# Kernel tuning notes

Hardware: AMD Instinct MI355X
Metric: run time of the kernel (lower is better)

Reference implementation:

```python
import jax, jax.numpy as jnp
import numpy as np

N = 200_000   # nodes per component
E = 400_000   # directed edges per component
F_IN = 32     # raw node features
H = 96        # hidden_dim / GatedGraphConv out_channels
L = 6         # num_layers inside GatedGraphConv
B = 4096      # number of molecules (graphs) in batch
FC = 4 * H    # 384


def _gru_cell(m, h, w_ih, w_hh, b_ih, b_hh):
    # torch.nn.GRUCell math; w_* are [3H, H], b_* are [3H]
    gi = m @ w_ih.T + b_ih
    gh = h @ w_hh.T + b_hh
    i_r, i_z, i_n = jnp.split(gi, 3, axis=1)
    h_r, h_z, h_n = jnp.split(gh, 3, axis=1)
    r = jax.nn.sigmoid(i_r + h_r)
    z = jax.nn.sigmoid(i_z + h_z)
    n = jnp.tanh(i_n + r * h_n)
    return (1.0 - z) * n + z * h


def _gated_graph_conv(x, edge_index, W, w_ih, w_hh, b_ih, b_hh):
    n_nodes = x.shape[0]
    h = jnp.pad(x, ((0, 0), (0, H - x.shape[1])))  # pad features to H
    src, dst = edge_index[0], edge_index[1]        # message flows src -> dst
    for i in range(L):
        m = h @ W[i]                                # [N, H]
        agg = jax.ops.segment_sum(m[src], dst, num_segments=n_nodes)
        h = _gru_cell(agg, h, w_ih, w_hh, b_ih, b_hh)
    return h


def _pool_component(x, edge_index, batch, W, w_ih, w_hh, b_ih, b_hh):
    h = jax.nn.relu(_gated_graph_conv(x, edge_index, W, w_ih, w_hh, b_ih, b_hh))
    sums = jax.ops.segment_sum(h, batch, num_segments=B)
    cnt = jax.ops.segment_sum(jnp.ones((h.shape[0], 1), h.dtype), batch, num_segments=B)
    return sums / jnp.maximum(cnt, 1.0)            # global_mean_pool -> [B, H]


def setup_inputs() -> dict:
    key = jax.random.key(0)
    ks = jax.random.split(key, 16)
    d = {}
    for i in range(3):
        c = str(i + 1)
        kx, ke, kb = jax.random.split(ks[i], 3)
        d['x' + c] = jax.random.normal(kx, (N, F_IN), jnp.float32)
        d['edge_index' + c] = jax.random.randint(ke, (2, E), 0, N)
        d['batch' + c] = jnp.sort(jax.random.randint(kb, (N,), 0, B))
        kw = jax.random.split(ks[3 + i], 5)
        d['W' + c] = jax.random.normal(kw[0], (L, H, H), jnp.float32) * 0.05
        d['wih' + c] = jax.random.normal(kw[1], (3 * H, H), jnp.float32) * 0.05
        d['whh' + c] = jax.random.normal(kw[2], (3 * H, H), jnp.float32) * 0.05
        d['bih' + c] = jax.random.normal(kw[3], (3 * H,), jnp.float32) * 0.05
        d['bhh' + c] = jax.random.normal(kw[4], (3 * H,), jnp.float32) * 0.05
    kf = jax.random.split(ks[7], 6)
    d['fc1_w'] = jax.random.normal(kf[0], (FC, FC * 4), jnp.float32) * 0.05
    d['fc1_b'] = jnp.zeros((FC * 4,), jnp.float32)
    d['fc2_w'] = jax.random.normal(kf[1], (FC * 4, FC), jnp.float32) * 0.05
    d['fc2_b'] = jnp.zeros((FC,), jnp.float32)
    d['fc3_w'] = jax.random.normal(kf[2], (FC, 3), jnp.float32) * 0.05
    d['fc3_b'] = jnp.zeros((3,), jnp.float32)
    return d


def reference(x1, edge_index1, batch1, x2, edge_index2, batch2, x3, edge_index3, batch3,
              W1, wih1, whh1, bih1, bhh1,
              W2, wih2, whh2, bih2, bhh2,
              W3, wih3, whh3, bih3, bhh3,
              fc1_w, fc1_b, fc2_w, fc2_b, fc3_w, fc3_b):
    g1 = _pool_component(x1, edge_index1, batch1, W1, wih1, whh1, bih1, bhh1)
    g2 = _pool_component(x2, edge_index2, batch2, W2, wih2, whh2, bih2, bhh2)
    g3 = _pool_component(x3, edge_index3, batch3, W3, wih3, whh3, bih3, bhh3)
    xx = g1 * g2 * g3
    x = jnp.concatenate((g1, g2, g3, xx), axis=1)   # [B, 4H]
    x = jax.nn.relu(x @ fc1_w + fc1_b)              # dropout is identity (eval)
    x = jax.nn.relu(x @ fc2_w + fc2_b)
    return x @ fc3_w + fc3_b                        # [B, 3]
```

## Files before the change

kernel.cpp:

```cpp
#include <hip/hip_runtime.h>
#include <math.h>

#define NN_ 200000
#define EE_ 400000
#define HH  96
#define LL  6
#define BB  4096
#define NT_ 12500
#define SCAN_B 1024
#define NB_SCAN 196

typedef short s8v __attribute__((ext_vector_type(8)));
typedef float f4v __attribute__((ext_vector_type(4)));
typedef float f2v __attribute__((ext_vector_type(2)));

static inline int cdiv(int a, int b) { return (a + b - 1) / b; }

__device__ __forceinline__ float sigmoidf_(float x) { return 1.0f / (1.0f + __expf(-x)); }
__device__ __forceinline__ float tanhf_(float x) { return 1.0f - 2.0f / (__expf(2.0f * x) + 1.0f); }
__device__ __forceinline__ unsigned short f2bf(float x) {
    unsigned u = __float_as_uint(x);
    unsigned r = u + 0x7FFF + ((u >> 16) & 1);
    return (unsigned short)(r >> 16);
}
__device__ __forceinline__ float bf2f(unsigned short u) {
    return __uint_as_float(((unsigned)u) << 16);
}
__device__ __forceinline__ s8v load_bf8(const float* __restrict__ p) {
    float4 v0 = *(const float4*)p;
    float4 v1 = *(const float4*)(p + 4);
    s8v r;
    r[0] = (short)f2bf(v0.x); r[1] = (short)f2bf(v0.y);
    r[2] = (short)f2bf(v0.z); r[3] = (short)f2bf(v0.w);
    r[4] = (short)f2bf(v1.x); r[5] = (short)f2bf(v1.y);
    r[6] = (short)f2bf(v1.z); r[7] = (short)f2bf(v1.w);
    return r;
}

__device__ __forceinline__ void accu_(f2v& a, unsigned u) {
    a[0] += __uint_as_float(u << 16);
    a[1] += __uint_as_float(u & 0xFFFF0000u);
}
__device__ __forceinline__ void acc_row_(f2v* ag2, const uint4& u, int ks) {
    accu_(ag2[ks * 4 + 0], u.x); accu_(ag2[ks * 4 + 1], u.y);
    accu_(ag2[ks * 4 + 2], u.z); accu_(ag2[ks * 4 + 3], u.w);
}

__global__ void packB_k(const float* __restrict__ B, unsigned short* __restrict__ Bp,
                        int K, int N)
{
    int idx = blockIdx.x * 256 + threadIdx.x;
    if (idx >= K * N) return;
    int k = idx / N, n = idx % N;
    Bp[(((size_t)(k >> 5) * N + n) * 4 + ((k >> 3) & 3)) * 8 + (k & 7)] = f2bf(B[idx]);
}

__global__ void packWp_k(const float* __restrict__ W, unsigned short* __restrict__ Wp)
{
    int idx = blockIdx.x * 256 + threadIdx.x;
    if (idx >= LL * 6 * 3 * 64 * 8) return;
    int j    = idx & 7;
    int lane = (idx >> 3) & 63;
    int rest = idx >> 9;
    int ks = rest % 3;
    int jb = (rest / 3) % 6;
    int l  = rest / 18;
    int quad = lane >> 4, lc = lane & 15;
    int k = ks * 32 + quad * 8 + j;
    int n = jb * 16 + lc;
    Wp[idx] = f2bf(W[(size_t)l * 9216 + (size_t)k * 96 + n]);
}

__global__ void packWgc_k(const float* __restrict__ wih, const float* __restrict__ whh,
                          unsigned short* __restrict__ Wgc)
{
    int idx = blockIdx.x * 256 + threadIdx.x;
    if (idx >= 6 * 18 * 64 * 8) return;
    int j    = idx & 7;
    int lane = (idx >> 3) & 63;
    int rest = idx >> 9;
    int ksb = rest % 18;
    int jb  = rest / 18;
    int quad = lane >> 4, lc = lane & 15;
    int g, ks;
    if (ksb < 6)       { g = 0; ks = ksb; }
    else if (ksb < 12) { g = 1; ks = ksb - 6; }
    else if (ksb < 15) { g = 2; ks = ksb - 12; }
    else               { g = 3; ks = ksb - 12; }
    int k = ks * 32 + quad * 8 + j;
    int n = g * 96 + jb * 16 + lc;
    float v;
    if (n < 192) {
        v = (k < 96) ? wih[(size_t)n * 96 + k] : whh[(size_t)n * 96 + (k - 96)];
    } else if (n < 288) {
        int jj = n - 192;
        v = wih[(size_t)(192 + jj) * 96 + k];
    } else {
        int jj = n - 288;
        v = whh[(size_t)(192 + jj) * 96 + (k - 96)];
    }
    Wgc[idx] = f2bf(v);
}

__global__ void bpack_k(const float* __restrict__ bih, const float* __restrict__ bhh,
                        float* __restrict__ bs)
{
    int j = threadIdx.x;
    if (j >= 96) return;
    bs[j]        = bih[j] + bhh[j];
    bs[96 + j]   = bih[96 + j] + bhh[96 + j];
    bs[192 + j]  = bih[192 + j];
    bs[288 + j]  = bhh[192 + j];
}

__global__ void pad_k(const float* __restrict__ x, unsigned short* __restrict__ hbf)
{
    int idx = blockIdx.x * 256 + threadIdx.x;
    if (idx >= NN_ * HH) return;
    int n = idx / HH, j = idx % HH;
    float v = (j < 32) ? x[n * 32 + j] : 0.f;
    hbf[idx] = f2bf(v);
}

__global__ void deg_k(const int* __restrict__ ei, int* __restrict__ deg)
{
    int e = blockIdx.x * 256 + threadIdx.x;
    if (e >= EE_) return;
    atomicAdd(&deg[ei[EE_ + e]], 1);
}

__global__ __launch_bounds__(SCAN_B) void scan1_k(
    const int* __restrict__ deg, int* __restrict__ rp, int* __restrict__ bsum)
{
    __shared__ int sh[SCAN_B];
    int i = blockIdx.x * SCAN_B + threadIdx.x;
    int v = (i < NN_) ? deg[i] : 0;
    sh[threadIdx.x] = v;
    __syncthreads();
    for (int off = 1; off < SCAN_B; off <<= 1) {
        int t = (threadIdx.x >= off) ? sh[threadIdx.x - off] : 0;
        __syncthreads();
        sh[threadIdx.x] += t;
        __syncthreads();
    }
    if (i < NN_) rp[i] = sh[threadIdx.x] - v;
    if (threadIdx.x == SCAN_B - 1) bsum[blockIdx.x] = sh[threadIdx.x];
}

__global__ __launch_bounds__(256) void scan2_k(int* __restrict__ bsum)
{
    __shared__ int sh[256];
    int v = (threadIdx.x < NB_SCAN) ? bsum[threadIdx.x] : 0;
    sh[threadIdx.x] = v;
    __syncthreads();
    for (int off = 1; off < 256; off <<= 1) {
        int t = (threadIdx.x >= off) ? sh[threadIdx.x - off] : 0;
        __syncthreads();
        sh[threadIdx.x] += t;
        __syncthreads();
    }
    if (threadIdx.x < NB_SCAN) bsum[threadIdx.x] = sh[threadIdx.x] - v;
}

__global__ void scan3_k(int* __restrict__ rp, const int* __restrict__ bsum,
                        int* __restrict__ cur)
{
    int i = blockIdx.x * 256 + threadIdx.x;
    if (i < NN_) {
        int r = rp[i] + bsum[i / SCAN_B];
        rp[i] = r;
        cur[i] = r;
    }
    if (i == 0) rp[NN_] = EE_;
}

__global__ void fill_k(const int* __restrict__ ei, int* __restrict__ cur,
                       int* __restrict__ srcs)
{
    int e = blockIdx.x * 256 + threadIdx.x;
    if (e >= EE_) return;
    int s = ei[e];
    int d = ei[EE_ + e];
    int pos = atomicAdd(&cur[d], 1);
    srcs[pos] = s * 192;
}

__global__ void brp_k(const int* __restrict__ bat, int* __restrict__ rpb)
{
    int i = blockIdx.x * 256 + threadIdx.x;
    if (i >= NN_) return;
    int b = bat[i];
    if (i == 0) {
        for (int q = 0; q <= b; q++) rpb[q] = 0;
    } else {
        int p = bat[i - 1];
        for (int q = p + 1; q <= b; q++) rpb[q] = i;
    }
    if (i == NN_ - 1) {
        for (int q = b + 1; q <= BB; q++) rpb[q] = NN_;
    }
}

__global__ __launch_bounds__(128) void agg_k(
    const int* __restrict__ rp, const int* __restrict__ srcs,
    const unsigned short* __restrict__ hbf,
    unsigned short* __restrict__ aggbf)
{
    int tid  = threadIdx.x;
    int wave = tid >> 6;
    int lane = tid & 63;
    int quad = lane >> 4;
    int lc   = lane & 15;
    int nT0  = blockIdx.x * 4 + wave * 2;

    const char* gbase = (const char*)hbf + quad * 16;

    #pragma unroll
    for (int t = 0; t < 2; t++) {
        int node = (nT0 + t) * 16 + lc;
        f2v ag2[12];
        #pragma unroll
        for (int i = 0; i < 12; i++) ag2[i] = (f2v){0.f, 0.f};
        int e = rp[node], e1 = rp[node + 1];
        for (; e < e1; e++) {
            const char* r = gbase + srcs[e];
            uint4 u0 = *(const uint4*)r;
            uint4 u1 = *(const uint4*)(r + 64);
            uint4 u2 = *(const uint4*)(r + 128);
            acc_row_(ag2, u0, 0); acc_row_(ag2, u1, 1); acc_row_(ag2, u2, 2);
        }
        #pragma unroll
        for (int ks = 0; ks < 3; ks++) {
            unsigned q0 = (unsigned)f2bf(ag2[ks * 4 + 0][0]) | ((unsigned)f2bf(ag2[ks * 4 + 0][1]) << 16);
            unsigned q1 = (unsigned)f2bf(ag2[ks * 4 + 1][0]) | ((unsigned)f2bf(ag2[ks * 4 + 1][1]) << 16);
            unsigned q2 = (unsigned)f2bf(ag2[ks * 4 + 2][0]) | ((unsigned)f2bf(ag2[ks * 4 + 2][1]) << 16);
            unsigned q3 = (unsigned)f2bf(ag2[ks * 4 + 3][0]) | ((unsigned)f2bf(ag2[ks * 4 + 3][1]) << 16);
            *(uint4*)(aggbf + (size_t)node * 96 + ks * 32 + quad * 8) =
                make_uint4(q0, q1, q2, q3);
        }
    }
}

__global__ __launch_bounds__(512) void gru_k(
    const unsigned short* __restrict__ aggbf,
    const unsigned short* __restrict__ Wp,
    const unsigned short* __restrict__ Wgc,
    const float* __restrict__ bs,
    const unsigned short* __restrict__ hbf_prev,
    unsigned short* __restrict__ hbf_next,
    float* __restrict__ h,
    int writeH)
{
    __shared__ unsigned short lw[27648];
    __shared__ unsigned short as_[8][32][36];
    int tid  = threadIdx.x;
    int half = blockIdx.y;

    {
        const uint4* src = (const uint4*)Wgc + (size_t)half * 3456;
        uint4* dst = (uint4*)lw;
        #pragma unroll
        for (int it = 0; it < 7; it++) {
            int i = it * 512 + tid;
            if (i < 3456) dst[i] = src[i];
        }
    }
    __syncthreads();

    int wave = tid >> 6;
    int lane = tid & 63;
    int quad = lane >> 4;
    int lc   = lane & 15;
    int nT0  = blockIdx.x * 16 + wave * 2;

    bool val[2];
    val[0] = (nT0 + 0) < NT_;
    val[1] = (nT0 + 1) < NT_;

    s8v z8;
    #pragma unroll
    for (int q = 0; q < 8; q++) z8[q] = 0;

    s8v hg[2][3], dh[2][3];
    #pragma unroll
    for (int t = 0; t < 2; t++) {
        int node = (nT0 + t) * 16 + lc;
        #pragma unroll
        for (int ks = 0; ks < 3; ks++) {
            if (val[t]) {
                hg[t][ks] = *(const s8v*)(aggbf    + (size_t)node * 96 + ks * 32 + quad * 8);
                dh[t][ks] = *(const s8v*)(hbf_prev + (size_t)node * 96 + ks * 32 + quad * 8);
            } else {
                hg[t][ks] = z8;
                dh[t][ks] = z8;
            }
        }
    }

    s8v d[2][6];
    #pragma unroll
    for (int kb = 0; kb < 3; kb++) {
        #pragma unroll
        for (int jj = 0; jj < 2; jj++) {
            int jb = kb * 2 + jj;
            f4v a1[2] = {};
            #pragma unroll
            for (int ks = 0; ks < 3; ks++) {
                s8v w = *(const s8v*)(Wp + ((size_t)(jb * 3 + ks) * 64 + lane) * 8);
                a1[0] = __builtin_amdgcn_mfma_f32_16x16x32_bf16(w, hg[0][ks], a1[0], 0, 0, 0);
                a1[1] = __builtin_amdgcn_mfma_f32_16x16x32_bf16(w, hg[1][ks], a1[1], 0, 0, 0);
            }
            #pragma unroll
            for (int t = 0; t < 2; t++) {
                unsigned short o0 = f2bf(a1[t][0]), o1 = f2bf(a1[t][1]);
                unsigned short o2 = f2bf(a1[t][2]), o3 = f2bf(a1[t][3]);
                *(uint2*)&as_[wave][t * 16 + lc][jj * 16 + quad * 4] =
                    make_uint2((unsigned)o0 | ((unsigned)o1 << 16),
                               (unsigned)o2 | ((unsigned)o3 << 16));
            }
        }
        #pragma unroll
        for (int t = 0; t < 2; t++)
            d[t][kb] = *(const s8v*)&as_[wave][t * 16 + lc][quad * 8];
    }
    #pragma unroll
    for (int t = 0; t < 2; t++) {
        d[t][3] = dh[t][0]; d[t][4] = dh[t][1]; d[t][5] = dh[t][2];
    }

    for (int jbl = 0; jbl < 3; jbl++) {
        int jb = half * 3 + jbl;
        uint2 hu[2];
        #pragma unroll
        for (int t = 0; t < 2; t++) {
            if (val[t])
                hu[t] = *(const uint2*)(hbf_prev + (size_t)((nT0 + t) * 16 + lc) * 96 + jb * 16 + quad * 4);
            else
                hu[t] = make_uint2(0u, 0u);
        }
        f4v acc[2][4] = {};
        const unsigned short* wj = lw + (size_t)jbl * 18 * 512 + (size_t)lane * 8;
        #pragma unroll
        for (int ks = 0; ks < 6; ks++) {
            s8v w = *(const s8v*)(wj + ks * 512);
            acc[0][0] = __builtin_amdgcn_mfma_f32_16x16x32_bf16(w, d[0][ks], acc[0][0], 0, 0, 0);
            acc[1][0] = __builtin_amdgcn_mfma_f32_16x16x32_bf16(w, d[1][ks], acc[1][0], 0, 0, 0);
        }
        #pragma unroll
        for (int ks = 0; ks < 6; ks++) {
            s8v w = *(const s8v*)(wj + (6 + ks) * 512);
            acc[0][1] = __builtin_amdgcn_mfma_f32_16x16x32_bf16(w, d[0][ks], acc[0][1], 0, 0, 0);
            acc[1][1] = __builtin_amdgcn_mfma_f32_16x16x32_bf16(w, d[1][ks], acc[1][1], 0, 0, 0);
        }
        #pragma unroll
        for (int ks = 0; ks < 6; ks++) {
            s8v w = *(const s8v*)(wj + (12 + ks) * 512);
            int g = (ks < 3) ? 2 : 3;
            acc[0][g] = __builtin_amdgcn_mfma_f32_16x16x32_bf16(w, d[0][ks], acc[0][g], 0, 0, 0);
            acc[1][g] = __builtin_amdgcn_mfma_f32_16x16x32_bf16(w, d[1][ks], acc[1][g], 0, 0, 0);
        }
        const float* bp = bs + jb * 16 + quad * 4;
        float4 br  = *(const float4*)(bp);
        float4 bz  = *(const float4*)(bp + 96);
        float4 bin = *(const float4*)(bp + 192);
        float4 bhn = *(const float4*)(bp + 288);
        float brv[4]  = {br.x, br.y, br.z, br.w};
        float bzv[4]  = {bz.x, bz.y, bz.z, bz.w};
        float binv[4] = {bin.x, bin.y, bin.z, bin.w};
        float bhnv[4] = {bhn.x, bhn.y, bhn.z, bhn.w};
        #pragma unroll
        for (int t = 0; t < 2; t++) {
            if (!val[t]) continue;
            int node = (nT0 + t) * 16 + lc;
            float hv[4];
            hv[0] = bf2f((unsigned short)(hu[t].x & 0xFFFF));
            hv[1] = bf2f((unsigned short)(hu[t].x >> 16));
            hv[2] = bf2f((unsigned short)(hu[t].y & 0xFFFF));
            hv[3] = bf2f((unsigned short)(hu[t].y >> 16));
            float out[4];
            #pragma unroll
            for (int i = 0; i < 4; i++) {
                float rg = sigmoidf_(acc[t][0][i] + brv[i]);
                float zg = sigmoidf_(acc[t][1][i] + bzv[i]);
                float nn = tanhf_(acc[t][2][i] + binv[i] + rg * (acc[t][3][i] + bhnv[i]));
                out[i] = (1.f - zg) * nn + zg * hv[i];
            }
            unsigned short q0 = f2bf(out[0]), q1 = f2bf(out[1]);
            unsigned short q2 = f2bf(out[2]), q3 = f2bf(out[3]);
            *(uint2*)(hbf_next + (size_t)node * 96 + jb * 16 + quad * 4) =
                make_uint2((unsigned)q0 | ((unsigned)q1 << 16),
                           (unsigned)q2 | ((unsigned)q3 << 16));
            if (writeH) {
                float* hp = h + (size_t)node * 96 + jb * 16 + quad * 4;
                *(float4*)hp = make_float4(out[0], out[1], out[2], out[3]);
            }
        }
    }
}

__global__ __launch_bounds__(128) void pool_csr_k(
    const float* __restrict__ h, const int* __restrict__ rpb, float* __restrict__ g)
{
    int b = blockIdx.x;
    int j = threadIdx.x;
    if (j >= 96) return;
    int n0 = rpb[b], n1 = rpb[b + 1];
    float s = 0.f;
    for (int n = n0; n < n1; n++) s += fmaxf(h[(size_t)n * 96 + j], 0.f);
    float c = (float)(n1 - n0);
    g[(size_t)b * 96 + j] = s / fmaxf(c, 1.f);
}

__global__ void feat_k(const float* __restrict__ g1, const float* __restrict__ g2,
                       const float* __restrict__ g3, float* __restrict__ feat)
{
    int idx = blockIdx.x * 256 + threadIdx.x;
    if (idx >= BB * HH) return;
    int b = idx / HH, j = idx % HH;
    float a = g1[idx], bb = g2[idx], c = g3[idx];
    float* f = feat + (size_t)b * 384;
    f[j]       = a;
    f[96 + j]  = bb;
    f[192 + j] = c;
    f[288 + j] = a * bb * c;
}

__global__ __launch_bounds__(256) void gemm_mlp_mfma(
    const float* __restrict__ A, const unsigned short* __restrict__ Bp,
    const float* __restrict__ bias, float* __restrict__ C,
    int K, int N, int doRelu)
{
    int wave = threadIdx.x >> 6;
    int lane = threadIdx.x & 63;
    int quad = lane >> 4;
    int lc   = lane & 15;
    int rowA = blockIdx.y * 16 + lc;
    int colb = blockIdx.x * 128 + wave * 32;

    f4v acc[2] = {};
    for (int ks = 0; ks < K / 32; ks++) {
        s8v a = load_bf8(A + (size_t)rowA * K + ks * 32 + quad * 8);
        #pragma unroll
        for (int t = 0; t < 2; t++) {
            int n = colb + t * 16 + lc;
            s8v b = *(const s8v*)(Bp + ((size_t)(ks * N + n) * 4 + quad) * 8);
            acc[t] = __builtin_amdgcn_mfma_f32_16x16x32_bf16(a, b, acc[t], 0, 0, 0);
        }
    }
    int rowD = blockIdx.y * 16 + quad * 4;
    #pragma unroll
    for (int t = 0; t < 2; t++) {
        int n = colb + t * 16 + lc;
        float bv = bias[n];
        #pragma unroll
        for (int r = 0; r < 4; r++) {
            float v = acc[t][r] + bv;
            if (doRelu) v = fmaxf(v, 0.f);
            C[(size_t)(rowD + r) * N + n] = v;
        }
    }
}

__global__ __launch_bounds__(256) void fc3_k(const float* __restrict__ t2,
                                             const float* __restrict__ w,
                                             const float* __restrict__ bias,
                                             float* __restrict__ out)
{
    int wave = threadIdx.x >> 6;
    int lane = threadIdx.x & 63;
    int b = blockIdx.x * 4 + wave;
    const float* row = t2 + (size_t)b * 384;
    float a0 = 0.f, a1 = 0.f, a2 = 0.f;
    #pragma unroll
    for (int kk = 0; kk < 6; kk++) {
        int k = kk * 64 + lane;
        float x = row[k];
        a0 += x * w[k * 3 + 0];
        a1 += x * w[k * 3 + 1];
        a2 += x * w[k * 3 + 2];
    }
    #pragma unroll
    for (int off = 32; off > 0; off >>= 1) {
        a0 += __shfl_down(a0, off);
        a1 += __shfl_down(a1, off);
        a2 += __shfl_down(a2, off);
    }
    if (lane == 0) {
        out[b * 3 + 0] = a0 + bias[0];
        out[b * 3 + 1] = a1 + bias[1];
        out[b * 3 + 2] = a2 + bias[2];
    }
}

extern "C" void kernel_launch(void* const* d_in, const int* in_sizes, int n_in,
                              void* d_out, int out_size, void* d_ws, size_t ws_size,
                              hipStream_t stream)
{
    float* ws    = (float*)d_ws;
    float* h     = ws;
    float* hbfAF = h + (size_t)NN_ * HH;
    float* hbfBF = hbfAF + (size_t)NN_ * HH / 2;
    float* aggF  = hbfBF + (size_t)NN_ * HH / 2;
    float* wpF   = aggF + (size_t)NN_ * HH / 2;
    float* wgpF  = wpF + 27648;
    float* fc1pF = wgpF + 36864;
    float* fc2pF = fc1pF + 294912;
    float* g3    = fc2pF + 294912;
    int*   rp    = (int*)(g3 + 3 * (size_t)BB * HH);
    int*   srcs  = rp + 200064;
    int*   deg   = srcs + 400000;
    int*   cur   = deg + 200000;
    int*   bsum  = cur + 200000;
    int*   rpb   = bsum + 256;
    float* bs    = (float*)(rpb + 4097) + 1;

    unsigned short* hbfA = (unsigned short*)hbfAF;
    unsigned short* hbfB = (unsigned short*)hbfBF;
    unsigned short* agg  = (unsigned short*)aggF;
    unsigned short* Wp   = (unsigned short*)wpF;
    unsigned short* Wgc  = (unsigned short*)wgpF;
    unsigned short* fc1p = (unsigned short*)fc1pF;
    unsigned short* fc2p = (unsigned short*)fc2pF;

    float* feat = h;
    float* t1   = h + 2 * 1024 * 1024;
    float* t2   = h + 9 * 1024 * 1024;

    for (int c = 0; c < 3; c++) {
        const float* x   = (const float*)d_in[c * 8 + 0];
        const int*   ei  = (const int*)  d_in[c * 8 + 1];
        const int*   bat = (const int*)  d_in[c * 8 + 2];
        const float* W   = (const float*)d_in[c * 8 + 3];
        const float* wih = (const float*)d_in[c * 8 + 4];
        const float* whh = (const float*)d_in[c * 8 + 5];
        const float* bih = (const float*)d_in[c * 8 + 6];
        const float* bhh = (const float*)d_in[c * 8 + 7];

        hipMemsetAsync(deg, 0, NN_ * sizeof(int), stream);
        deg_k<<<cdiv(EE_, 256), 256, 0, stream>>>(ei, deg);
        scan1_k<<<NB_SCAN, SCAN_B, 0, stream>>>(deg, rp, bsum);
        scan2_k<<<1, 256, 0, stream>>>(bsum);
        scan3_k<<<cdiv(NN_, 256), 256, 0, stream>>>(rp, bsum, cur);
        fill_k<<<cdiv(EE_, 256), 256, 0, stream>>>(ei, cur, srcs);
        brp_k<<<cdiv(NN_, 256), 256, 0, stream>>>(bat, rpb);

        packWp_k<<<cdiv(LL * 6 * 3 * 64 * 8, 256), 256, 0, stream>>>(W, Wp);
        packWgc_k<<<cdiv(6 * 18 * 64 * 8, 256), 256, 0, stream>>>(wih, whh, Wgc);
        bpack_k<<<1, 128, 0, stream>>>(bih, bhh, bs);
        pad_k<<<cdiv(NN_ * HH, 256), 256, 0, stream>>>(x, hbfA);

        unsigned short* pb[2] = {hbfA, hbfB};
        for (int l = 0; l < LL; l++) {
            agg_k<<<NN_ / 64, 128, 0, stream>>>(rp, srcs, pb[l & 1], agg);
            gru_k<<<dim3(cdiv(NT_, 16), 2), 512, 0, stream>>>(
                agg, Wp + (size_t)l * 9216, Wgc, bs, pb[l & 1], pb[(l + 1) & 1],
                h, (l == LL - 1) ? 1 : 0);
        }

        pool_csr_k<<<BB, 128, 0, stream>>>(h, rpb, g3 + (size_t)c * BB * HH);
    }

    const float* fc1_w = (const float*)d_in[24];
    const float* fc1_b = (const float*)d_in[25];
    const float* fc2_w = (const float*)d_in[26];
    const float* fc2_b = (const float*)d_in[27];
    const float* fc3_w = (const float*)d_in[28];
    const float* fc3_b = (const float*)d_in[29];

    packB_k<<<cdiv(384 * 1536, 256), 256, 0, stream>>>(fc1_w, fc1p, 384, 1536);
    packB_k<<<cdiv(1536 * 384, 256), 256, 0, stream>>>(fc2_w, fc2p, 1536, 384);

    feat_k<<<cdiv(BB * HH, 256), 256, 0, stream>>>(
        g3, g3 + (size_t)BB * HH, g3 + 2 * (size_t)BB * HH, feat);
    gemm_mlp_mfma<<<dim3(1536 / 128, BB / 16), 256, 0, stream>>>(
        feat, fc1p, fc1_b, t1, 384, 1536, 1);
    gemm_mlp_mfma<<<dim3(384 / 128, BB / 16), 256, 0, stream>>>(
        t1, fc2p, fc2_b, t2, 1536, 384, 1);
    fc3_k<<<BB / 4, 256, 0, stream>>>(t2, fc3_w, fc3_b, (float*)d_out);
}
```

Measured before the change: 2.487 ms.

## Store node features in six 16-column planes instead of row-major rows

```diff
diff --git a/kernel.cpp b/kernel.cpp
--- a/kernel.cpp
+++ b/kernel.cpp
@@ -7,6 +7,7 @@
 #define LL  6
 #define BB  4096
 #define NT_ 12500
+#define PLE (NN_ * 16)
 #define SCAN_B 1024
 #define NB_SCAN 196
 
@@ -116,8 +117,12 @@
 __global__ void pad_k(const float* __restrict__ x, unsigned short* __restrict__ hbf)
 {
     int idx = blockIdx.x * 256 + threadIdx.x;
-    if (idx >= NN_ * HH) return;
-    int n = idx / HH, j = idx % HH;
+    if (idx >= 6 * PLE) return;
+    int p  = idx / PLE;
+    int r  = idx - p * PLE;
+    int n  = r >> 4;
+    int jj = r & 15;
+    int j  = p * 16 + jj;
     float v = (j < 32) ? x[n * 32 + j] : 0.f;
     hbf[idx] = f2bf(v);
 }
@@ -182,7 +187,7 @@
     int s = ei[e];
     int d = ei[EE_ + e];
     int pos = atomicAdd(&cur[d], 1);
-    srcs[pos] = s * 192;
+    srcs[pos] = s * 32;
 }
 
 __global__ void brp_k(const int* __restrict__ bat, int* __restrict__ rpb)
@@ -212,8 +217,11 @@
     int quad = lane >> 4;
     int lc   = lane & 15;
     int nT0  = blockIdx.x * 4 + wave * 2;
-
-    const char* gbase = (const char*)hbf + quad * 16;
+    int q2 = quad >> 1, q1 = quad & 1;
+
+    const char* g0 = (const char*)(hbf + (size_t)(0 + q2) * PLE) + q1 * 16;
+    const char* g1 = (const char*)(hbf + (size_t)(2 + q2) * PLE) + q1 * 16;
+    const char* g2 = (const char*)(hbf + (size_t)(4 + q2) * PLE) + q1 * 16;
 
     #pragma unroll
     for (int t = 0; t < 2; t++) {
@@ -223,20 +231,20 @@
         for (int i = 0; i < 12; i++) ag2[i] = (f2v){0.f, 0.f};
         int e = rp[node], e1 = rp[node + 1];
         for (; e < e1; e++) {
-            const char* r = gbase + srcs[e];
-            uint4 u0 = *(const uint4*)r;
-            uint4 u1 = *(const uint4*)(r + 64);
-            uint4 u2 = *(const uint4*)(r + 128);
+            int off = srcs[e];
+            uint4 u0 = *(const uint4*)(g0 + off);
+            uint4 u1 = *(const uint4*)(g1 + off);
+            uint4 u2 = *(const uint4*)(g2 + off);
             acc_row_(ag2, u0, 0); acc_row_(ag2, u1, 1); acc_row_(ag2, u2, 2);
         }
         #pragma unroll
         for (int ks = 0; ks < 3; ks++) {
-            unsigned q0 = (unsigned)f2bf(ag2[ks * 4 + 0][0]) | ((unsigned)f2bf(ag2[ks * 4 + 0][1]) << 16);
-            unsigned q1 = (unsigned)f2bf(ag2[ks * 4 + 1][0]) | ((unsigned)f2bf(ag2[ks * 4 + 1][1]) << 16);
-            unsigned q2 = (unsigned)f2bf(ag2[ks * 4 + 2][0]) | ((unsigned)f2bf(ag2[ks * 4 + 2][1]) << 16);
-            unsigned q3 = (unsigned)f2bf(ag2[ks * 4 + 3][0]) | ((unsigned)f2bf(ag2[ks * 4 + 3][1]) << 16);
-            *(uint4*)(aggbf + (size_t)node * 96 + ks * 32 + quad * 8) =
-                make_uint4(q0, q1, q2, q3);
+            unsigned p0 = (unsigned)f2bf(ag2[ks * 4 + 0][0]) | ((unsigned)f2bf(ag2[ks * 4 + 0][1]) << 16);
+            unsigned p1 = (unsigned)f2bf(ag2[ks * 4 + 1][0]) | ((unsigned)f2bf(ag2[ks * 4 + 1][1]) << 16);
+            unsigned p2 = (unsigned)f2bf(ag2[ks * 4 + 2][0]) | ((unsigned)f2bf(ag2[ks * 4 + 2][1]) << 16);
+            unsigned p3 = (unsigned)f2bf(ag2[ks * 4 + 3][0]) | ((unsigned)f2bf(ag2[ks * 4 + 3][1]) << 16);
+            *(uint4*)(aggbf + (size_t)(2 * ks + q2) * PLE + (size_t)node * 16 + q1 * 8) =
+                make_uint4(p0, p1, p2, p3);
         }
     }
 }
@@ -272,6 +280,7 @@
     int quad = lane >> 4;
     int lc   = lane & 15;
     int nT0  = blockIdx.x * 16 + wave * 2;
+    int q2 = quad >> 1, q1 = quad & 1;
 
     bool val[2];
     val[0] = (nT0 + 0) < NT_;
@@ -287,9 +296,10 @@
         int node = (nT0 + t) * 16 + lc;
         #pragma unroll
         for (int ks = 0; ks < 3; ks++) {
+            size_t base = (size_t)(2 * ks + q2) * PLE + (size_t)node * 16 + q1 * 8;
             if (val[t]) {
-                hg[t][ks] = *(const s8v*)(aggbf    + (size_t)node * 96 + ks * 32 + quad * 8);
-                dh[t][ks] = *(const s8v*)(hbf_prev + (size_t)node * 96 + ks * 32 + quad * 8);
+                hg[t][ks] = *(const s8v*)(aggbf    + base);
+                dh[t][ks] = *(const s8v*)(hbf_prev + base);
             } else {
                 hg[t][ks] = z8;
                 dh[t][ks] = z8;
@@ -334,7 +344,8 @@
         #pragma unroll
         for (int t = 0; t < 2; t++) {
             if (val[t])
-                hu[t] = *(const uint2*)(hbf_prev + (size_t)((nT0 + t) * 16 + lc) * 96 + jb * 16 + quad * 4);
+                hu[t] = *(const uint2*)(hbf_prev + (size_t)jb * PLE +
+                                        (size_t)((nT0 + t) * 16 + lc) * 16 + quad * 4);
             else
                 hu[t] = make_uint2(0u, 0u);
         }
@@ -385,11 +396,11 @@
                 float nn = tanhf_(acc[t][2][i] + binv[i] + rg * (acc[t][3][i] + bhnv[i]));
                 out[i] = (1.f - zg) * nn + zg * hv[i];
             }
-            unsigned short q0 = f2bf(out[0]), q1 = f2bf(out[1]);
-            unsigned short q2 = f2bf(out[2]), q3 = f2bf(out[3]);
-            *(uint2*)(hbf_next + (size_t)node * 96 + jb * 16 + quad * 4) =
-                make_uint2((unsigned)q0 | ((unsigned)q1 << 16),
-                           (unsigned)q2 | ((unsigned)q3 << 16));
+            unsigned short q0 = f2bf(out[0]), q1_ = f2bf(out[1]);
+            unsigned short q2_ = f2bf(out[2]), q3 = f2bf(out[3]);
+            *(uint2*)(hbf_next + (size_t)jb * PLE + (size_t)node * 16 + quad * 4) =
+                make_uint2((unsigned)q0 | ((unsigned)q1_ << 16),
+                           (unsigned)q2_ | ((unsigned)q3 << 16));
             if (writeH) {
                 float* hp = h + (size_t)node * 96 + jb * 16 + quad * 4;
                 *(float4*)hp = make_float4(out[0], out[1], out[2], out[3]);
@@ -547,7 +558,7 @@
         packWp_k<<<cdiv(LL * 6 * 3 * 64 * 8, 256), 256, 0, stream>>>(W, Wp);
         packWgc_k<<<cdiv(6 * 18 * 64 * 8, 256), 256, 0, stream>>>(wih, whh, Wgc);
         bpack_k<<<1, 128, 0, stream>>>(bih, bhh, bs);
-        pad_k<<<cdiv(NN_ * HH, 256), 256, 0, stream>>>(x, hbfA);
+        pad_k<<<cdiv(6 * PLE, 256), 256, 0, stream>>>(x, hbfA);
 
         unsigned short* pb[2] = {hbfA, hbfB};
         for (int l = 0; l < LL; l++) {
```

After: 3.209 ms. +29.1%, slower.

## Fold per-layer W into GRU input weights to skip the message GEMM

Applied to the files above, without the earlier changes.

```diff
diff --git a/kernel.cpp b/kernel.cpp
--- a/kernel.cpp
+++ b/kernel.cpp
@@ -55,30 +55,33 @@
     Bp[(((size_t)(k >> 5) * N + n) * 4 + ((k >> 3) & 3)) * 8 + (k & 7)] = f2bf(B[idx]);
 }
 
-__global__ void packWp_k(const float* __restrict__ W, unsigned short* __restrict__ Wp)
+__global__ void wfuse_k(const float* __restrict__ W, const float* __restrict__ wih,
+                        float* __restrict__ wf)
 {
     int idx = blockIdx.x * 256 + threadIdx.x;
-    if (idx >= LL * 6 * 3 * 64 * 8) return;
-    int j    = idx & 7;
-    int lane = (idx >> 3) & 63;
-    int rest = idx >> 9;
-    int ks = rest % 3;
-    int jb = (rest / 3) % 6;
-    int l  = rest / 18;
-    int quad = lane >> 4, lc = lane & 15;
-    int k = ks * 32 + quad * 8 + j;
-    int n = jb * 16 + lc;
-    Wp[idx] = f2bf(W[(size_t)l * 9216 + (size_t)k * 96 + n]);
-}
-
-__global__ void packWgc_k(const float* __restrict__ wih, const float* __restrict__ whh,
-                          unsigned short* __restrict__ Wgc)
+    if (idx >= LL * 96 * 288) return;
+    int l = idx / (96 * 288);
+    int r = idx - l * 96 * 288;
+    int k = r / 288;
+    int g = r - k * 288;
+    const float* wr = W + (size_t)l * 9216 + (size_t)k * 96;
+    const float* vr = wih + (size_t)g * 96;
+    float s = 0.f;
+    #pragma unroll 8
+    for (int j = 0; j < 96; j++) s += wr[j] * vr[j];
+    wf[idx] = s;
+}
+
+__global__ void packWgf_k(const float* __restrict__ wf, const float* __restrict__ whh,
+                          unsigned short* __restrict__ Wgf)
 {
     int idx = blockIdx.x * 256 + threadIdx.x;
-    if (idx >= 6 * 18 * 64 * 8) return;
-    int j    = idx & 7;
-    int lane = (idx >> 3) & 63;
-    int rest = idx >> 9;
+    if (idx >= LL * 6 * 18 * 64 * 8) return;
+    int l = idx / 55296;
+    int r = idx - l * 55296;
+    int j    = r & 7;
+    int lane = (r >> 3) & 63;
+    int rest = r >> 9;
     int ksb = rest % 18;
     int jb  = rest / 18;
     int quad = lane >> 4, lc = lane & 15;
@@ -90,16 +93,13 @@
     int k = ks * 32 + quad * 8 + j;
     int n = g * 96 + jb * 16 + lc;
     float v;
-    if (n < 192) {
-        v = (k < 96) ? wih[(size_t)n * 96 + k] : whh[(size_t)n * 96 + (k - 96)];
-    } else if (n < 288) {
-        int jj = n - 192;
-        v = wih[(size_t)(192 + jj) * 96 + k];
+    if (n < 288) {
+        v = (k < 96) ? wf[(size_t)l * 27648 + (size_t)k * 288 + n]
+                     : whh[(size_t)n * 96 + (k - 96)];
     } else {
-        int jj = n - 288;
-        v = whh[(size_t)(192 + jj) * 96 + (k - 96)];
-    }
-    Wgc[idx] = f2bf(v);
+        v = whh[(size_t)(192 + (n - 288)) * 96 + (k - 96)];
+    }
+    Wgf[idx] = f2bf(v);
 }
 
 __global__ void bpack_k(const float* __restrict__ bih, const float* __restrict__ bhh,
@@ -243,8 +243,7 @@
 
 __global__ __launch_bounds__(512) void gru_k(
     const unsigned short* __restrict__ aggbf,
-    const unsigned short* __restrict__ Wp,
-    const unsigned short* __restrict__ Wgc,
+    const unsigned short* __restrict__ Wgf,
     const float* __restrict__ bs,
     const unsigned short* __restrict__ hbf_prev,
     unsigned short* __restrict__ hbf_next,
@@ -252,12 +251,11 @@
     int writeH)
 {
     __shared__ unsigned short lw[27648];
-    __shared__ unsigned short as_[8][32][36];
     int tid  = threadIdx.x;
-    int half = blockIdx.y;
+    int part = blockIdx.y;
 
     {
-        const uint4* src = (const uint4*)Wgc + (size_t)half * 3456;
+        const uint4* src = (const uint4*)Wgf + (size_t)part * 3456;
         uint4* dst = (uint4*)lw;
         #pragma unroll
         for (int it = 0; it < 7; it++) {
@@ -281,55 +279,24 @@
     #pragma unroll
     for (int q = 0; q < 8; q++) z8[q] = 0;
 
-    s8v hg[2][3], dh[2][3];
+    s8v d[2][6];
     #pragma unroll
     for (int t = 0; t < 2; t++) {
         int node = (nT0 + t) * 16 + lc;
         #pragma unroll
         for (int ks = 0; ks < 3; ks++) {
             if (val[t]) {
-                hg[t][ks] = *(const s8v*)(aggbf    + (size_t)node * 96 + ks * 32 + quad * 8);
-                dh[t][ks] = *(const s8v*)(hbf_prev + (size_t)node * 96 + ks * 32 + quad * 8);
+                d[t][ks]     = *(const s8v*)(aggbf    + (size_t)node * 96 + ks * 32 + quad * 8);
+                d[t][3 + ks] = *(const s8v*)(hbf_prev + (size_t)node * 96 + ks * 32 + quad * 8);
             } else {
-                hg[t][ks] = z8;
-                dh[t][ks] = z8;
+                d[t][ks]     = z8;
+                d[t][3 + ks] = z8;
             }
         }
     }
 
-    s8v d[2][6];
-    #pragma unroll
-    for (int kb = 0; kb < 3; kb++) {
-        #pragma unroll
-        for (int jj = 0; jj < 2; jj++) {
-            int jb = kb * 2 + jj;
-            f4v a1[2] = {};
-            #pragma unroll
-            for (int ks = 0; ks < 3; ks++) {
-                s8v w = *(const s8v*)(Wp + ((size_t)(jb * 3 + ks) * 64 + lane) * 8);
-                a1[0] = __builtin_amdgcn_mfma_f32_16x16x32_bf16(w, hg[0][ks], a1[0], 0, 0, 0);
-                a1[1] = __builtin_amdgcn_mfma_f32_16x16x32_bf16(w, hg[1][ks], a1[1], 0, 0, 0);
-            }
-            #pragma unroll
-            for (int t = 0; t < 2; t++) {
-                unsigned short o0 = f2bf(a1[t][0]), o1 = f2bf(a1[t][1]);
-                unsigned short o2 = f2bf(a1[t][2]), o3 = f2bf(a1[t][3]);
-                *(uint2*)&as_[wave][t * 16 + lc][jj * 16 + quad * 4] =
-                    make_uint2((unsigned)o0 | ((unsigned)o1 << 16),
-                               (unsigned)o2 | ((unsigned)o3 << 16));
-            }
-        }
-        #pragma unroll
-        for (int t = 0; t < 2; t++)
-            d[t][kb] = *(const s8v*)&as_[wave][t * 16 + lc][quad * 8];
-    }
-    #pragma unroll
-    for (int t = 0; t < 2; t++) {
-        d[t][3] = dh[t][0]; d[t][4] = dh[t][1]; d[t][5] = dh[t][2];
-    }
-
     for (int jbl = 0; jbl < 3; jbl++) {
-        int jb = half * 3 + jbl;
+        int jb = part * 3 + jbl;
         uint2 hu[2];
         #pragma unroll
         for (int t = 0; t < 2; t++) {
@@ -501,9 +468,9 @@
     float* hbfAF = h + (size_t)NN_ * HH;
     float* hbfBF = hbfAF + (size_t)NN_ * HH / 2;
     float* aggF  = hbfBF + (size_t)NN_ * HH / 2;
-    float* wpF   = aggF + (size_t)NN_ * HH / 2;
-    float* wgpF  = wpF + 27648;
-    float* fc1pF = wgpF + 36864;
+    float* wfF   = aggF + (size_t)NN_ * HH / 2;
+    float* wgfF  = wfF + 165888;
+    float* fc1pF = wgfF + 165888;
     float* fc2pF = fc1pF + 294912;
     float* g3    = fc2pF + 294912;
     int*   rp    = (int*)(g3 + 3 * (size_t)BB * HH);
@@ -517,8 +484,7 @@
     unsigned short* hbfA = (unsigned short*)hbfAF;
     unsigned short* hbfB = (unsigned short*)hbfBF;
     unsigned short* agg  = (unsigned short*)aggF;
-    unsigned short* Wp   = (unsigned short*)wpF;
-    unsigned short* Wgc  = (unsigned short*)wgpF;
+    unsigned short* Wgf  = (unsigned short*)wgfF;
     unsigned short* fc1p = (unsigned short*)fc1pF;
     unsigned short* fc2p = (unsigned short*)fc2pF;
 
@@ -544,8 +510,8 @@
         fill_k<<<cdiv(EE_, 256), 256, 0, stream>>>(ei, cur, srcs);
         brp_k<<<cdiv(NN_, 256), 256, 0, stream>>>(bat, rpb);
 
-        packWp_k<<<cdiv(LL * 6 * 3 * 64 * 8, 256), 256, 0, stream>>>(W, Wp);
-        packWgc_k<<<cdiv(6 * 18 * 64 * 8, 256), 256, 0, stream>>>(wih, whh, Wgc);
+        wfuse_k<<<cdiv(LL * 96 * 288, 256), 256, 0, stream>>>(W, wih, wfF);
+        packWgf_k<<<cdiv(LL * 6 * 18 * 64 * 8, 256), 256, 0, stream>>>(wfF, whh, Wgf);
         bpack_k<<<1, 128, 0, stream>>>(bih, bhh, bs);
         pad_k<<<cdiv(NN_ * HH, 256), 256, 0, stream>>>(x, hbfA);
 
@@ -553,7 +519,7 @@
         for (int l = 0; l < LL; l++) {
             agg_k<<<NN_ / 64, 128, 0, stream>>>(rp, srcs, pb[l & 1], agg);
             gru_k<<<dim3(cdiv(NT_, 16), 2), 512, 0, stream>>>(
-                agg, Wp + (size_t)l * 9216, Wgc, bs, pb[l & 1], pb[(l + 1) & 1],
+                agg, Wgf + (size_t)l * 55296, bs, pb[l & 1], pb[(l + 1) & 1],
                 h, (l == LL - 1) ? 1 : 0);
         }
 
```

Measured after the change: 2.288 ms. 8.0% less time.
